# Kernel tuning notes

Measured on AMD Instinct MI355X. Metric: run time of the kernel, lower is better.

Reference implementation:

```python
import jax, jax.numpy as jnp
import numpy as np

B, C1, C2, H, W = 8, 256, 512, 56, 56

def setup_inputs() -> dict:
    key = jax.random.key(0)
    k1, k2, k3, k4, k5 = jax.random.split(key, 5)
    return {
        "x1": jax.random.normal(k1, (B, C1, H, W), dtype=jnp.float32),
        "x2": jax.random.normal(k2, (B, C2, H, W), dtype=jnp.float32),
        "W_proj": jax.random.normal(k3, (C1, C2), dtype=jnp.float32) * (1.0 / np.sqrt(C2)),
        "b_proj": jax.random.normal(k4, (C1,), dtype=jnp.float32) * 0.01,
        "gamma": jax.random.normal(k5, (1,), dtype=jnp.float32) * 0.1,
    }

def reference(x1, x2, W_proj, b_proj, gamma):
    b, c, h, w = x1.shape
    n = h * w
    # 1x1 conv projection C2 -> C1
    x2p = jnp.einsum('oc,bchw->bohw', W_proj, x2) + b_proj[None, :, None, None]
    query = x1.reshape(b, c, n).transpose(0, 2, 1)   # [B, N, C]
    key_ = x2p.reshape(b, c, n)                      # [B, C, N]
    value = x2p.reshape(b, c, n).transpose(0, 2, 1)  # [B, N, C]
    energy = jnp.einsum('bnc,bcm->bnm', query, key_)  # [B, N, N]
    # inverted-energy softmax: max - energy, then softmax over last dim
    energy_new = jnp.max(energy, axis=-1, keepdims=True) - energy
    attention = jax.nn.softmax(energy_new, axis=-1)
    out = jnp.einsum('bnm,bmc->bnc', attention, value)  # [B, N, C]
    out = out.transpose(0, 2, 1).reshape(b, c, h, w)
    return gamma[0] * out + x1
```

## Files before the change

### kernel.cpp

```cpp
#include <hip/hip_runtime.h>
#include <hip/hip_bf16.h>

#define C1 256
#define C2 512
#define NSP 3136
#define NT 98

typedef __attribute__((ext_vector_type(8))) short bf16x8;
typedef __attribute__((ext_vector_type(4))) float f32x4;

__device__ __forceinline__ ushort f2b(float f) {
  __hip_bfloat16 h = __float2bfloat16(f);
  return *reinterpret_cast<ushort*>(&h);
}
__device__ __forceinline__ float b2f(ushort u) {
  union { unsigned int i; float f; } v; v.i = ((unsigned int)u) << 16; return v.f;
}
__device__ __forceinline__ void gload16(const ushort* g, ushort* l) {
  __builtin_amdgcn_global_load_lds(
      (const __attribute__((address_space(1))) void*)g,
      (__attribute__((address_space(3))) void*)l, 16, 0, 0);
}
__device__ __forceinline__ void block_bar() {
  asm volatile("" ::: "memory");
  __builtin_amdgcn_s_barrier();
  asm volatile("" ::: "memory");
}

__global__ __launch_bounds__(256) void k_wtf(const float* __restrict__ W,
                                             ushort* __restrict__ Wf) {
  int ot = blockIdx.x;
  int tid = threadIdx.x;
  int lane = tid & 63, l15 = lane & 15, g = (lane >> 4) & 3;
  int cc0 = (tid >> 6) * 4;
  const float* src = W + (size_t)(ot * 16 + l15) * C2 + g * 8;
#pragma unroll
  for (int k = 0; k < 4; k++) {
    int cc = cc0 + k;
    float4 u0 = *reinterpret_cast<const float4*>(src + cc * 32);
    float4 u1 = *reinterpret_cast<const float4*>(src + cc * 32 + 4);
    bf16x8 v;
    v[0] = (short)f2b(u0.x); v[1] = (short)f2b(u0.y);
    v[2] = (short)f2b(u0.z); v[3] = (short)f2b(u0.w);
    v[4] = (short)f2b(u1.x); v[5] = (short)f2b(u1.y);
    v[6] = (short)f2b(u1.z); v[7] = (short)f2b(u1.w);
    *reinterpret_cast<bf16x8*>(Wf + ((size_t)(ot * 16 + cc)) * 512 + lane * 8) = v;
  }
}

__global__ __launch_bounds__(256) void k_x1t(const float* __restrict__ x1,
                                             ushort* __restrict__ x1t) {
  __shared__ float t[32][33];
  int b = blockIdx.z;
  int n0 = blockIdx.x * 32;
  int c0 = blockIdx.y * 32;
  int tid = threadIdx.x;
  int r = tid >> 3, q = (tid & 7) * 4;
  const float* src = x1 + ((size_t)b * C1 + (c0 + r)) * NSP + n0 + q;
  float4 v = *reinterpret_cast<const float4*>(src);
  t[r][q] = v.x; t[r][q + 1] = v.y; t[r][q + 2] = v.z; t[r][q + 3] = v.w;
  __syncthreads();
  ushort4 o;
  o.x = f2b(t[q + 0][r]); o.y = f2b(t[q + 1][r]);
  o.z = f2b(t[q + 2][r]); o.w = f2b(t[q + 3][r]);
  *reinterpret_cast<ushort4*>(x1t + ((size_t)b * NSP + n0 + r) * C1 + c0 + q) = o;
}

__global__ __launch_bounds__(256) void k_x2f(const float* __restrict__ x2,
                                             ushort* __restrict__ x2f) {
  __shared__ float t[32][33];
  int b = blockIdx.z;
  int n0 = blockIdx.x * 32;
  int cc = blockIdx.y;
  int c0 = cc * 32;
  int tid = threadIdx.x;
  int r = tid >> 3, q = (tid & 7) * 4;
  const float* src = x2 + ((size_t)b * C2 + (c0 + r)) * NSP + n0 + q;
  float4 v = *reinterpret_cast<const float4*>(src);
  t[r][q] = v.x; t[r][q + 1] = v.y; t[r][q + 2] = v.z; t[r][q + 3] = v.w;
  __syncthreads();
  int l15 = tid & 15, g = (tid >> 4) & 3, sub = tid >> 6;
  int ntl = sub & 1, ih = sub >> 1;
  int nl = ntl * 16 + l15;
  int cl = g * 8 + ih * 4;
  ushort4 o;
  o.x = f2b(t[cl + 0][nl]); o.y = f2b(t[cl + 1][nl]);
  o.z = f2b(t[cl + 2][nl]); o.w = f2b(t[cl + 3][nl]);
  int nt16 = (n0 >> 4) + ntl;
  *reinterpret_cast<ushort4*>(
      x2f + (((size_t)b * 196 + nt16) * 16 + cc) * 512 + (size_t)(tid & 63) * 8 + ih * 4) = o;
}

__global__ __launch_bounds__(256) void k_proj(const ushort* __restrict__ Wf,
    const ushort* __restrict__ x2f, const float* __restrict__ bias,
    ushort* __restrict__ Kf, ushort* __restrict__ Vf) {
  __shared__ __align__(16) ushort WL[2][8][512];
  __shared__ __align__(16) ushort XL[2][4][512];
  int bid = blockIdx.x;
  int b = bid & 7;
  int tq = bid >> 3;
  int oh = tq & 1;
  int nt = tq >> 1;
  int tid = threadIdx.x;
  int w = tid >> 6, lane = tid & 63, l15 = lane & 15, g = lane >> 4;
  int wq = w >> 1, wn = w & 1;
  int ot0 = oh * 8;
  int nt0 = nt * 4;

  auto stage = [&](int buf, int cc) {
#pragma unroll
    for (int j = 0; j < 3; j++) {
      int chunk = w * 3 + j;
      if (chunk < 8) {
        gload16(Wf + ((size_t)(ot0 + chunk) * 16 + cc) * 512 + lane * 8,
                &WL[buf][chunk][0]);
      } else {
        gload16(x2f + (((size_t)b * 196 + nt0 + (chunk - 8)) * 16 + cc) * 512 + lane * 8,
                &XL[buf][chunk - 8][0]);
      }
    }
  };

  f32x4 zero = {0.f, 0.f, 0.f, 0.f};
  f32x4 acc[4][2];
#pragma unroll
  for (int a = 0; a < 4; a++)
#pragma unroll
    for (int v = 0; v < 2; v++) acc[a][v] = zero;

  stage(0, 0);
  __syncthreads();

  for (int cc = 0; cc < 16; ++cc) {
    int cur = cc & 1;
    if (cc < 15) stage(cur ^ 1, cc + 1);
    bf16x8 A[4], Bf[2];
#pragma unroll
    for (int a = 0; a < 4; a++)
      A[a] = *reinterpret_cast<const bf16x8*>(&WL[cur][wq * 4 + a][lane * 8]);
#pragma unroll
    for (int v = 0; v < 2; v++)
      Bf[v] = *reinterpret_cast<const bf16x8*>(&XL[cur][wn * 2 + v][lane * 8]);
#pragma unroll
    for (int a = 0; a < 4; a++)
#pragma unroll
      for (int v = 0; v < 2; v++)
        acc[a][v] = __builtin_amdgcn_mfma_f32_16x16x32_bf16(A[a], Bf[v], acc[a][v], 0, 0, 0);
    __syncthreads();
  }

  int obase = oh * 128 + wq * 64;
  float4 bias4[4];
#pragma unroll
  for (int a = 0; a < 4; a++)
    bias4[a] = *reinterpret_cast<const float4*>(&bias[obase + a * 16 + g * 4]);

  int gk = (g & 1) * 4;
#pragma unroll
  for (int a = 0; a < 4; a++) {
    int laneK = (((2 * a + (g >> 1)) & 3) << 4) | l15;
    size_t oK = (size_t)(oh * 4 + wq * 2 + (a >> 1));
#pragma unroll
    for (int v = 0; v < 2; v++) {
      int nK = nt * 4 + wn * 2 + v;
      ushort4 st;
      st.x = f2b(acc[a][v][0] + bias4[a].x);
      st.y = f2b(acc[a][v][1] + bias4[a].y);
      st.z = f2b(acc[a][v][2] + bias4[a].z);
      st.w = f2b(acc[a][v][3] + bias4[a].w);
      *reinterpret_cast<ushort4*>(
          Kf + ((((size_t)b * 196 + nK) * 8 + oK) * 64 + laneK) * 8 + gk) = st;
    }
  }
  int nV = nt * 2 + wn;
#pragma unroll
  for (int v = 0; v < 2; v++) {
    int gv = ((v * 2 + (l15 >> 3)) & 3) << 4;
    int iV = l15 & 7;
#pragma unroll
    for (int a = 0; a < 4; a++) {
      int cs = oh * 8 + wq * 4 + a;
      size_t basev = ((((size_t)b * 98 + nV) * 16 + cs) * 64 + gv) * 8 + iV;
      const float* bp4 = reinterpret_cast<const float*>(&bias4[a]);
#pragma unroll
      for (int r = 0; r < 4; r++)
        Vf[basev + (size_t)(g * 4 + r) * 8] = f2b(acc[a][v][r] + bp4[r]);
    }
  }
}

__global__ __launch_bounds__(256, 3) void k_attn_s(
    const ushort* __restrict__ x1t, const ushort* __restrict__ Kf,
    const ushort* __restrict__ Vf,
    ushort* __restrict__ Po, float* __restrict__ Mv, float* __restrict__ Lv) {
  __shared__ __align__(16) ushort Kt[2][8192];
  __shared__ __align__(16) ushort Vt[8192];
  __shared__ __align__(16) ushort Plds[4][16][36];
  int bid = blockIdx.x;
  int x = bid & 7;
  int j = bid >> 3;
  int s = (4802 * j) / 96;
  int e = (4802 * (j + 1)) / 96;
  int tid = threadIdx.x;
  int w = tid >> 6;
  int lane = tid & 63;
  int l15 = lane & 15;
  int g = lane >> 4;
  int nloc = w * 16 + g * 4;

  const ushort* kg = Kf + (size_t)x * 196 * 8 * 512;
  const ushort* vg = Vf + (size_t)x * 98 * 16 * 512;
  int soff = w * 2048;

  f32x4 zero = {0.f, 0.f, 0.f, 0.f};
  f32x4 O[16];
  f32x4 O17 = zero;
  float M[4];
  bf16x8 qf[8];
  bf16x8 onesf;
#pragma unroll
  for (int i = 0; i < 8; i++) onesf[i] = (short)0x3F80;

  auto resetacc = [&]() {
#pragma unroll
    for (int i = 0; i < 16; i++) O[i] = zero;
    O17 = zero;
#pragma unroll
    for (int r = 0; r < 4; r++) M[r] = -3.0e38f;
  };
  auto loadQ = [&](int u) {
    const ushort* qb = x1t + ((size_t)x * NSP + u * 64 + w * 16 + l15) * C1 + g * 8;
#pragma unroll
    for (int cc = 0; cc < 8; cc++)
      qf[cc] = *reinterpret_cast<const bf16x8*>(qb + cc * 32);
  };

  int u = s / 98;
  int kv = s - u * 98;
  loadQ(u);
  resetacc();
  {
    const ushort* ks = kg + (size_t)kv * 8192 + soff + lane * 8;
#pragma unroll
    for (int jj = 0; jj < 4; ++jj) gload16(ks + jj * 512, &Kt[0][soff] + jj * 512);
  }
  asm volatile("s_waitcnt vmcnt(0)" ::: "memory");
  block_bar();

  int cur = 0;
  for (int i = s; i < e; ++i) {
    {
      const ushort* vs = vg + (size_t)kv * 8192 + soff + lane * 8;
#pragma unroll
      for (int jj = 0; jj < 4; ++jj) gload16(vs + jj * 512, &Vt[soff] + jj * 512);
    }
    asm volatile("" ::: "memory");
    if (i + 1 < e) {
      int kvn = (kv == 97) ? 0 : kv + 1;
      const ushort* ks = kg + (size_t)kvn * 8192 + soff + lane * 8;
#pragma unroll
      for (int jj = 0; jj < 4; ++jj) gload16(ks + jj * 512, &Kt[cur ^ 1][soff] + jj * 512);
    }
    asm volatile("" ::: "memory");

    f32x4 s0a = zero, s0b = zero, s1a = zero, s1b = zero;
    const ushort* kb = &Kt[cur][0];
    __builtin_amdgcn_s_setprio(1);
#pragma unroll
    for (int cc = 0; cc < 8; cc += 2) {
      bf16x8 k00 = *reinterpret_cast<const bf16x8*>(kb + ((size_t)cc * 64 + lane) * 8);
      bf16x8 k10 = *reinterpret_cast<const bf16x8*>(kb + ((size_t)(8 + cc) * 64 + lane) * 8);
      bf16x8 k01 = *reinterpret_cast<const bf16x8*>(kb + ((size_t)(cc + 1) * 64 + lane) * 8);
      bf16x8 k11 = *reinterpret_cast<const bf16x8*>(kb + ((size_t)(9 + cc) * 64 + lane) * 8);
      s0a = __builtin_amdgcn_mfma_f32_16x16x32_bf16(qf[cc], k00, s0a, 0, 0, 0);
      s1a = __builtin_amdgcn_mfma_f32_16x16x32_bf16(qf[cc], k10, s1a, 0, 0, 0);
      s0b = __builtin_amdgcn_mfma_f32_16x16x32_bf16(qf[cc + 1], k01, s0b, 0, 0, 0);
      s1b = __builtin_amdgcn_mfma_f32_16x16x32_bf16(qf[cc + 1], k11, s1b, 0, 0, 0);
    }
    __builtin_amdgcn_s_setprio(0);

    float a0[4], a1[4], tmax[4];
#pragma unroll
    for (int r = 0; r < 4; r++) {
      a0[r] = -(s0a[r] + s0b[r]);
      a1[r] = -(s1a[r] + s1b[r]);
      float mx = fmaxf(a0[r], a1[r]);
      mx = fmaxf(mx, __shfl_xor(mx, 1));
      mx = fmaxf(mx, __shfl_xor(mx, 2));
      mx = fmaxf(mx, __shfl_xor(mx, 4));
      mx = fmaxf(mx, __shfl_xor(mx, 8));
      tmax[r] = mx;
    }
    float d01 = fmaxf(tmax[0] - M[0], tmax[1] - M[1]);
    float d23 = fmaxf(tmax[2] - M[2], tmax[3] - M[3]);
    if (__any(fmaxf(d01, d23) > 3.0f)) {
      float scv[4];
#pragma unroll
      for (int r = 0; r < 4; r++) {
        float nm = fmaxf(M[r], tmax[r]);
        scv[r] = __expf(M[r] - nm);
        M[r] = nm;
      }
#pragma unroll
      for (int i2 = 0; i2 < 16; i2++) {
#pragma unroll
        for (int r = 0; r < 4; r++) O[i2][r] *= scv[r];
      }
#pragma unroll
      for (int r = 0; r < 4; r++) O17[r] *= scv[r];
    }
#pragma unroll
    for (int r = 0; r < 4; r++) {
      float p0 = __expf(a0[r] - M[r]);
      float p1 = __expf(a1[r] - M[r]);
      Plds[w][g * 4 + r][l15] = f2b(p0);
      Plds[w][g * 4 + r][16 + l15] = f2b(p1);
    }

    if (i + 1 < e) { asm volatile("s_waitcnt vmcnt(4)" ::: "memory"); }
    else           { asm volatile("s_waitcnt vmcnt(0)" ::: "memory"); }
    block_bar();

    asm volatile("s_waitcnt lgkmcnt(0)" ::: "memory");
    bf16x8 pf = *reinterpret_cast<const bf16x8*>(&Plds[w][l15][g * 8]);
    __builtin_amdgcn_s_setprio(1);
#pragma unroll
    for (int cs = 0; cs < 16; ++cs) {
      bf16x8 vf = *reinterpret_cast<const bf16x8*>(&Vt[0] + ((size_t)cs * 64 + lane) * 8);
      O[cs] = __builtin_amdgcn_mfma_f32_16x16x32_bf16(pf, vf, O[cs], 0, 0, 0);
    }
    O17 = __builtin_amdgcn_mfma_f32_16x16x32_bf16(pf, onesf, O17, 0, 0, 0);
    __builtin_amdgcn_s_setprio(0);

    asm volatile("s_waitcnt vmcnt(0)" ::: "memory");
    block_bar();
    cur ^= 1;

    if ((i + 1 == e) || (kv == 97)) {
      int firstj = (9408 * u + 95) / 4802;
      int slot = (x * 49 + u) * 3 + (j - firstj);
#pragma unroll
      for (int cs = 0; cs < 16; cs++) {
        int c = cs * 16 + l15;
        ushort4 st;
        st.x = f2b(O[cs][0]); st.y = f2b(O[cs][1]);
        st.z = f2b(O[cs][2]); st.w = f2b(O[cs][3]);
        *reinterpret_cast<ushort4*>(Po + ((size_t)slot * 256 + c) * 64 + nloc) = st;
      }
      if (l15 == 0) {
#pragma unroll
        for (int r = 0; r < 4; r++) {
          Mv[(size_t)slot * 64 + nloc + r] = M[r];
          Lv[(size_t)slot * 64 + nloc + r] = O17[r];
        }
      }
      if (i + 1 < e && kv == 97) { u += 1; loadQ(u); resetacc(); }
    }
    kv = (kv == 97) ? 0 : kv + 1;
  }
}

__global__ __launch_bounds__(256) void k_comb3(
    const ushort* __restrict__ Po, const float* __restrict__ Mv,
    const float* __restrict__ Lv, const float* __restrict__ x1,
    const float* __restrict__ gamma, float* __restrict__ out) {
  int bid = blockIdx.x;
  int x = bid & 7;
  int u = bid >> 3;
  int tid = threadIdx.x;
  int n = tid & 63;
  int c0 = (tid >> 6) * 64;
  int firstj = (9408 * u + 95) / 4802;
  int lastj = (96 * (98 * u + 97) + 95) / 4802;
  int np = lastj - firstj + 1;
  size_t base = (size_t)(x * 49 + u) * 3;
  bool has2 = (np >= 3);

  float M0 = Mv[(base + 0) * 64 + n];
  float M1 = Mv[(base + 1) * 64 + n];
  float M2 = has2 ? Mv[(base + 2) * 64 + n] : -3.0e38f;
  float L0 = Lv[(base + 0) * 64 + n];
  float L1 = Lv[(base + 1) * 64 + n];
  float L2 = has2 ? Lv[(base + 2) * 64 + n] : 0.f;
  float Mg = fmaxf(fmaxf(M0, M1), M2);
  float w0 = __expf(M0 - Mg), w1 = __expf(M1 - Mg);
  float w2 = has2 ? __expf(M2 - Mg) : 0.f;
  float rl = gamma[0] / (w0 * L0 + w1 * L1 + w2 * L2);

  const ushort* p0 = Po + ((base + 0) * 256) * 64 + n;
  const ushort* p1 = Po + ((base + 1) * 256) * 64 + n;
  const ushort* p2 = Po + ((base + 2) * 256) * 64 + n;
  size_t ob = (size_t)x * C1 * NSP + u * 64 + n;
#pragma unroll 4
  for (int c = c0; c < c0 + 64; ++c) {
    float acc = w0 * b2f(p0[(size_t)c * 64]) + w1 * b2f(p1[(size_t)c * 64]);
    if (has2) acc += w2 * b2f(p2[(size_t)c * 64]);
    size_t idx = ob + (size_t)c * NSP;
    out[idx] = acc * rl + x1[idx];
  }
}

template<int SPLIT>
__global__ __launch_bounds__(256, 3) void k_attn(
    const ushort* __restrict__ x1t, const ushort* __restrict__ Kf,
    const ushort* __restrict__ Vf, const float* __restrict__ x1,
    const float* __restrict__ gamma, float* __restrict__ out,
    ushort* __restrict__ Po, float* __restrict__ Mv, float* __restrict__ Lv) {
  __shared__ __align__(16) ushort Kt[2][8192];
  __shared__ __align__(16) ushort Vt[8192];
  __shared__ __align__(16) ushort Plds[4][16][36];
  int bid = blockIdx.x;
  int b = bid & 7;
  int qt = SPLIT ? (bid >> 4) : (bid >> 3);
  int h = SPLIT ? ((bid >> 3) & 1) : 0;
  int t0 = h * 49;
  int t1 = SPLIT ? (t0 + 49) : NT;
  int tid = threadIdx.x;
  int w = tid >> 6;
  int lane = tid & 63;
  int l15 = lane & 15;
  int g = lane >> 4;
  int n0 = qt * 64 + w * 16;

  bf16x8 qf[8];
  const ushort* qb = x1t + ((size_t)b * NSP + n0 + l15) * C1 + g * 8;
#pragma unroll
  for (int cc = 0; cc < 8; cc++)
    qf[cc] = *reinterpret_cast<const bf16x8*>(qb + cc * 32);

  f32x4 zero = {0.f, 0.f, 0.f, 0.f};
  f32x4 O[16];
#pragma unroll
  for (int i = 0; i < 16; i++) O[i] = zero;
  f32x4 O17 = zero;
  float M[4];
#pragma unroll
  for (int r = 0; r < 4; r++) M[r] = -3.0e38f;
  bf16x8 onesf;
#pragma unroll
  for (int i = 0; i < 8; i++) onesf[i] = (short)0x3F80;

  const ushort* kg = Kf + (size_t)b * 196 * 8 * 512;
  const ushort* vg = Vf + (size_t)b * 98 * 16 * 512;
  int soff = w * 2048;

  {
    const ushort* ks = kg + (size_t)t0 * 8192 + soff + lane * 8;
#pragma unroll
    for (int jj = 0; jj < 4; ++jj) gload16(ks + jj * 512, &Kt[0][soff] + jj * 512);
  }
  asm volatile("s_waitcnt vmcnt(0)" ::: "memory");
  block_bar();

  int cur = 0;
  for (int t = t0; t < t1; ++t) {
    {
      const ushort* vs = vg + (size_t)t * 8192 + soff + lane * 8;
#pragma unroll
      for (int jj = 0; jj < 4; ++jj) gload16(vs + jj * 512, &Vt[soff] + jj * 512);
    }
    asm volatile("" ::: "memory");
    if (t + 1 < t1) {
      const ushort* ks = kg + (size_t)(t + 1) * 8192 + soff + lane * 8;
#pragma unroll
      for (int jj = 0; jj < 4; ++jj) gload16(ks + jj * 512, &Kt[cur ^ 1][soff] + jj * 512);
    }
    asm volatile("" ::: "memory");

    f32x4 s0a = zero, s0b = zero, s1a = zero, s1b = zero;
    const ushort* kb = &Kt[cur][0];
    __builtin_amdgcn_s_setprio(1);
#pragma unroll
    for (int cc = 0; cc < 8; cc += 2) {
      bf16x8 k00 = *reinterpret_cast<const bf16x8*>(kb + ((size_t)cc * 64 + lane) * 8);
      bf16x8 k10 = *reinterpret_cast<const bf16x8*>(kb + ((size_t)(8 + cc) * 64 + lane) * 8);
      bf16x8 k01 = *reinterpret_cast<const bf16x8*>(kb + ((size_t)(cc + 1) * 64 + lane) * 8);
      bf16x8 k11 = *reinterpret_cast<const bf16x8*>(kb + ((size_t)(9 + cc) * 64 + lane) * 8);
      s0a = __builtin_amdgcn_mfma_f32_16x16x32_bf16(qf[cc], k00, s0a, 0, 0, 0);
      s1a = __builtin_amdgcn_mfma_f32_16x16x32_bf16(qf[cc], k10, s1a, 0, 0, 0);
      s0b = __builtin_amdgcn_mfma_f32_16x16x32_bf16(qf[cc + 1], k01, s0b, 0, 0, 0);
      s1b = __builtin_amdgcn_mfma_f32_16x16x32_bf16(qf[cc + 1], k11, s1b, 0, 0, 0);
    }
    __builtin_amdgcn_s_setprio(0);

    float a0[4], a1[4], tmax[4];
#pragma unroll
    for (int r = 0; r < 4; r++) {
      a0[r] = -(s0a[r] + s0b[r]);
      a1[r] = -(s1a[r] + s1b[r]);
      float mx = fmaxf(a0[r], a1[r]);
      mx = fmaxf(mx, __shfl_xor(mx, 1));
      mx = fmaxf(mx, __shfl_xor(mx, 2));
      mx = fmaxf(mx, __shfl_xor(mx, 4));
      mx = fmaxf(mx, __shfl_xor(mx, 8));
      tmax[r] = mx;
    }
    float d01 = fmaxf(tmax[0] - M[0], tmax[1] - M[1]);
    float d23 = fmaxf(tmax[2] - M[2], tmax[3] - M[3]);
    if (__any(fmaxf(d01, d23) > 3.0f)) {
      float scv[4];
#pragma unroll
      for (int r = 0; r < 4; r++) {
        float nm = fmaxf(M[r], tmax[r]);
        scv[r] = __expf(M[r] - nm);
        M[r] = nm;
      }
#pragma unroll
      for (int i = 0; i < 16; i++) {
#pragma unroll
        for (int r = 0; r < 4; r++) O[i][r] *= scv[r];
      }
#pragma unroll
      for (int r = 0; r < 4; r++) O17[r] *= scv[r];
    }
#pragma unroll
    for (int r = 0; r < 4; r++) {
      float p0 = __expf(a0[r] - M[r]);
      float p1 = __expf(a1[r] - M[r]);
      Plds[w][g * 4 + r][l15] = f2b(p0);
      Plds[w][g * 4 + r][16 + l15] = f2b(p1);
    }

    if (t + 1 < t1) { asm volatile("s_waitcnt vmcnt(4)" ::: "memory"); }
    else            { asm volatile("s_waitcnt vmcnt(0)" ::: "memory"); }
    block_bar();

    asm volatile("s_waitcnt lgkmcnt(0)" ::: "memory");
    bf16x8 pf = *reinterpret_cast<const bf16x8*>(&Plds[w][l15][g * 8]);
    __builtin_amdgcn_s_setprio(1);
#pragma unroll
    for (int cs = 0; cs < 16; ++cs) {
      bf16x8 vf = *reinterpret_cast<const bf16x8*>(&Vt[0] + ((size_t)cs * 64 + lane) * 8);
      O[cs] = __builtin_amdgcn_mfma_f32_16x16x32_bf16(pf, vf, O[cs], 0, 0, 0);
    }
    O17 = __builtin_amdgcn_mfma_f32_16x16x32_bf16(pf, onesf, O17, 0, 0, 0);
    __builtin_amdgcn_s_setprio(0);

    asm volatile("s_waitcnt vmcnt(0)" ::: "memory");
    block_bar();
    cur ^= 1;
  }

  if (SPLIT) {
    int pb = bid;
    int nloc = w * 16 + g * 4;
#pragma unroll
    for (int cs = 0; cs < 16; cs++) {
      int c = cs * 16 + l15;
      ushort4 st;
      st.x = f2b(O[cs][0]); st.y = f2b(O[cs][1]);
      st.z = f2b(O[cs][2]); st.w = f2b(O[cs][3]);
      *reinterpret_cast<ushort4*>(Po + ((size_t)pb * 256 + c) * 64 + nloc) = st;
    }
    if (l15 == 0) {
#pragma unroll
      for (int r = 0; r < 4; r++) {
        Mv[(size_t)pb * 64 + nloc + r] = M[r];
        Lv[(size_t)pb * 64 + nloc + r] = O17[r];
      }
    }
  } else {
    float gm = gamma[0];
    float rl[4];
#pragma unroll
    for (int r = 0; r < 4; r++) rl[r] = gm / O17[r];
    size_t ob = (size_t)b * C1 * NSP + n0 + (size_t)g * 4;
#pragma unroll
    for (int cs = 0; cs < 16; cs++) {
      size_t idx = ob + (size_t)(cs * 16 + l15) * NSP;
      float4 x4 = *reinterpret_cast<const float4*>(&x1[idx]);
      float4 o4;
      o4.x = O[cs][0] * rl[0] + x4.x;
      o4.y = O[cs][1] * rl[1] + x4.y;
      o4.z = O[cs][2] * rl[2] + x4.z;
      o4.w = O[cs][3] * rl[3] + x4.w;
      *reinterpret_cast<float4*>(&out[idx]) = o4;
    }
  }
}

__global__ __launch_bounds__(256) void k_comb(
    const ushort* __restrict__ Po, const float* __restrict__ Mv,
    const float* __restrict__ Lv, const float* __restrict__ x1,
    const float* __restrict__ gamma, float* __restrict__ out) {
  int bid = blockIdx.x;
  int b = bid & 7;
  int qt = bid >> 3;
  int tid = threadIdx.x;
  int n = tid & 63;
  int c0 = (tid >> 6) * 64;
  int pb0 = qt * 16 + b;
  int pb1 = qt * 16 + 8 + b;
  int n0 = qt * 64;
  float M0 = Mv[(size_t)pb0 * 64 + n], M1 = Mv[(size_t)pb1 * 64 + n];
  float L0 = Lv[(size_t)pb0 * 64 + n], L1 = Lv[(size_t)pb1 * 64 + n];
  float Ms = fmaxf(M0, M1);
  float w0 = __expf(M0 - Ms), w1 = __expf(M1 - Ms);
  float rl = gamma[0] / (w0 * L0 + w1 * L1);
  const ushort* p0 = Po + (size_t)pb0 * 16384 + n;
  const ushort* p1 = Po + (size_t)pb1 * 16384 + n;
#pragma unroll 4
  for (int c = c0; c < c0 + 64; ++c) {
    float o0 = b2f(p0[(size_t)c * 64]);
    float o1 = b2f(p1[(size_t)c * 64]);
    size_t idx = ((size_t)b * C1 + c) * NSP + n0 + n;
    out[idx] = (w0 * o0 + w1 * o1) * rl + x1[idx];
  }
}

extern "C" void kernel_launch(void* const* d_in, const int* in_sizes, int n_in,
                              void* d_out, int out_size, void* d_ws, size_t ws_size,
                              hipStream_t stream) {
  const float* x1 = (const float*)d_in[0];
  const float* x2 = (const float*)d_in[1];
  const float* W = (const float*)d_in[2];
  const float* bp = (const float*)d_in[3];
  const float* gamma = (const float*)d_in[4];
  float* out = (float*)d_out;

  char* ws = (char*)d_ws;
  ushort* Wf = (ushort*)(ws + 0);
  ushort* x1t = (ushort*)(ws + 262144);
  ushort* Kf = (ushort*)(ws + 13107200);
  ushort* Vf = (ushort*)(ws + 25952256);
  ushort* Po = (ushort*)(ws + 38797312);
  float* Mv = (float*)(ws + 77332480);
  float* Lv = (float*)(ws + 77633536);
  ushort* Pof = (ushort*)(ws + 38797312);
  float* Mvf = (float*)(ws + 64487424);
  float* Lvf = (float*)(ws + 64688128);
  ushort* x2f = (ushort*)d_out;

  k_wtf<<<dim3(16), dim3(256), 0, stream>>>(W, Wf);
  k_x1t<<<dim3(98, 8, 8), dim3(256), 0, stream>>>(x1, x1t);
  k_x2f<<<dim3(98, 16, 8), dim3(256), 0, stream>>>(x2, x2f);
  k_proj<<<dim3(784), dim3(256), 0, stream>>>(Wf, x2f, bp, Kf, Vf);

  if (ws_size >= 77934592ULL) {
    k_attn_s<<<dim3(768), dim3(256), 0, stream>>>(x1t, Kf, Vf, Po, Mv, Lv);
    k_comb3<<<dim3(392), dim3(256), 0, stream>>>(Po, Mv, Lv, x1, gamma, out);
  } else if (ws_size >= 64888832ULL) {
    k_attn<1><<<dim3(784), dim3(256), 0, stream>>>(x1t, Kf, Vf, x1, gamma, out,
                                                   Pof, Mvf, Lvf);
    k_comb<<<dim3(392), dim3(256), 0, stream>>>(Pof, Mvf, Lvf, x1, gamma, out);
  } else {
    k_attn<0><<<dim3(392), dim3(256), 0, stream>>>(x1t, Kf, Vf, x1, gamma, out,
                                                   Pof, Mvf, Lvf);
  }
}
```

Baseline: 241.8 us.

## Add 128-row query tile stream-K attention kernel with four-way partial combine

Adds a new attention kernel in which each wave handles two 16-row query sub-tiles. Every K/V tile loaded into LDS is therefore reused across 128 query rows instead of 64, and the S and PV MFMA work per wave doubles. The work is split stream-K style over 512 blocks, with up to four partials combined by a new combine kernel. Occupancy drops to 2 blocks per CU because each wave carries twice the accumulator registers. The rescale threshold is raised to 8, and the old split/non-split fallback kernels are removed. The new path only runs when the workspace is large enough; otherwise the previous stream-K kernel is used.

```diff
diff --git a/kernel.cpp b/kernel.cpp
--- a/kernel.cpp
+++ b/kernel.cpp
@@ -189,6 +189,251 @@
   }
 }
 
+__global__ __launch_bounds__(256, 2) void k_attn_p(
+    const ushort* __restrict__ x1t, const ushort* __restrict__ Kf,
+    const ushort* __restrict__ Vf,
+    ushort* __restrict__ Po, float* __restrict__ Mv, float* __restrict__ Lv) {
+  __shared__ __align__(16) ushort Kt[2][8192];
+  __shared__ __align__(16) ushort Vt[8192];
+  __shared__ __align__(16) ushort Plds[4][2][16][36];
+  int bid = blockIdx.x;
+  int x = bid & 7;
+  int j = bid >> 3;
+  int s = (2450 * j) / 64;
+  int e = (2450 * (j + 1)) / 64;
+  int tid = threadIdx.x;
+  int w = tid >> 6;
+  int lane = tid & 63;
+  int l15 = lane & 15;
+  int g = lane >> 4;
+  int tp = w >> 1;
+  int h32 = w & 1;
+
+  const ushort* kg = Kf + (size_t)x * 196 * 8 * 512;
+  const ushort* vg = Vf + (size_t)x * 98 * 16 * 512;
+  int soff = w * 2048;
+
+  f32x4 zero = {0.f, 0.f, 0.f, 0.f};
+  f32x4 O0[16], O1[16];
+  f32x4 L0 = zero, L1 = zero;
+  float M[2][4];
+  bf16x8 qf0[8], qf1[8];
+  bf16x8 onesf;
+#pragma unroll
+  for (int i = 0; i < 8; i++) onesf[i] = (short)0x3F80;
+
+  auto resetacc = [&]() {
+#pragma unroll
+    for (int i = 0; i < 16; i++) { O0[i] = zero; O1[i] = zero; }
+    L0 = zero; L1 = zero;
+#pragma unroll
+    for (int r = 0; r < 4; r++) { M[0][r] = -3.0e38f; M[1][r] = -3.0e38f; }
+  };
+  auto loadQ = [&](int p_) {
+    int u_ = 2 * p_ + tp;
+    int rb = (u_ < 49) ? u_ * 64 + h32 * 32 : 0;
+    const ushort* q0 = x1t + ((size_t)x * NSP + rb + l15) * C1 + g * 8;
+    const ushort* q1 = x1t + ((size_t)x * NSP + rb + 16 + l15) * C1 + g * 8;
+#pragma unroll
+    for (int cc = 0; cc < 8; cc++) {
+      qf0[cc] = *reinterpret_cast<const bf16x8*>(q0 + cc * 32);
+      qf1[cc] = *reinterpret_cast<const bf16x8*>(q1 + cc * 32);
+    }
+  };
+
+  int p = s / 98;
+  int kv = s - p * 98;
+  loadQ(p);
+  resetacc();
+  {
+    const ushort* ks = kg + (size_t)kv * 8192 + soff + lane * 8;
+#pragma unroll
+    for (int jj = 0; jj < 4; ++jj) gload16(ks + jj * 512, &Kt[0][soff] + jj * 512);
+  }
+  asm volatile("s_waitcnt vmcnt(0)" ::: "memory");
+  block_bar();
+
+  int cur = 0;
+  for (int i = s; i < e; ++i) {
+    {
+      const ushort* vs = vg + (size_t)kv * 8192 + soff + lane * 8;
+#pragma unroll
+      for (int jj = 0; jj < 4; ++jj) gload16(vs + jj * 512, &Vt[soff] + jj * 512);
+    }
+    asm volatile("" ::: "memory");
+    if (i + 1 < e) {
+      int kvn = (kv == 97) ? 0 : kv + 1;
+      const ushort* ks = kg + (size_t)kvn * 8192 + soff + lane * 8;
+#pragma unroll
+      for (int jj = 0; jj < 4; ++jj) gload16(ks + jj * 512, &Kt[cur ^ 1][soff] + jj * 512);
+    }
+    asm volatile("" ::: "memory");
+
+    f32x4 sA0 = zero, sB0 = zero, sA1 = zero, sB1 = zero;
+    const ushort* kb = &Kt[cur][0];
+    __builtin_amdgcn_s_setprio(1);
+#pragma unroll
+    for (int cc = 0; cc < 8; ++cc) {
+      bf16x8 kl = *reinterpret_cast<const bf16x8*>(kb + ((size_t)cc * 64 + lane) * 8);
+      bf16x8 kh = *reinterpret_cast<const bf16x8*>(kb + ((size_t)(8 + cc) * 64 + lane) * 8);
+      sA0 = __builtin_amdgcn_mfma_f32_16x16x32_bf16(qf0[cc], kl, sA0, 0, 0, 0);
+      sB0 = __builtin_amdgcn_mfma_f32_16x16x32_bf16(qf0[cc], kh, sB0, 0, 0, 0);
+      sA1 = __builtin_amdgcn_mfma_f32_16x16x32_bf16(qf1[cc], kl, sA1, 0, 0, 0);
+      sB1 = __builtin_amdgcn_mfma_f32_16x16x32_bf16(qf1[cc], kh, sB1, 0, 0, 0);
+    }
+    __builtin_amdgcn_s_setprio(0);
+
+    float tmax[2][4];
+#pragma unroll
+    for (int qs = 0; qs < 2; qs++) {
+#pragma unroll
+      for (int r = 0; r < 4; r++) {
+        float a0 = qs ? -sA1[r] : -sA0[r];
+        float a1 = qs ? -sB1[r] : -sB0[r];
+        float mx = fmaxf(a0, a1);
+        mx = fmaxf(mx, __shfl_xor(mx, 1));
+        mx = fmaxf(mx, __shfl_xor(mx, 2));
+        mx = fmaxf(mx, __shfl_xor(mx, 4));
+        mx = fmaxf(mx, __shfl_xor(mx, 8));
+        tmax[qs][r] = mx;
+      }
+    }
+    float dm = -3.0e38f;
+#pragma unroll
+    for (int qs = 0; qs < 2; qs++)
+#pragma unroll
+      for (int r = 0; r < 4; r++) dm = fmaxf(dm, tmax[qs][r] - M[qs][r]);
+    if (__any(dm > 8.0f)) {
+      float sc0[4], sc1[4];
+#pragma unroll
+      for (int r = 0; r < 4; r++) {
+        float nm0 = fmaxf(M[0][r], tmax[0][r]);
+        float nm1 = fmaxf(M[1][r], tmax[1][r]);
+        sc0[r] = __expf(M[0][r] - nm0);
+        sc1[r] = __expf(M[1][r] - nm1);
+        M[0][r] = nm0; M[1][r] = nm1;
+      }
+#pragma unroll
+      for (int i2 = 0; i2 < 16; i2++) {
+#pragma unroll
+        for (int r = 0; r < 4; r++) { O0[i2][r] *= sc0[r]; O1[i2][r] *= sc1[r]; }
+      }
+#pragma unroll
+      for (int r = 0; r < 4; r++) { L0[r] *= sc0[r]; L1[r] *= sc1[r]; }
+    }
+#pragma unroll
+    for (int r = 0; r < 4; r++) {
+      Plds[w][0][g * 4 + r][l15]      = f2b(__expf(-sA0[r] - M[0][r]));
+      Plds[w][0][g * 4 + r][16 + l15] = f2b(__expf(-sB0[r] - M[0][r]));
+      Plds[w][1][g * 4 + r][l15]      = f2b(__expf(-sA1[r] - M[1][r]));
+      Plds[w][1][g * 4 + r][16 + l15] = f2b(__expf(-sB1[r] - M[1][r]));
+    }
+
+    if (i + 1 < e) { asm volatile("s_waitcnt vmcnt(4)" ::: "memory"); }
+    else           { asm volatile("s_waitcnt vmcnt(0)" ::: "memory"); }
+    block_bar();
+
+    asm volatile("s_waitcnt lgkmcnt(0)" ::: "memory");
+    bf16x8 pf0 = *reinterpret_cast<const bf16x8*>(&Plds[w][0][l15][g * 8]);
+    bf16x8 pf1 = *reinterpret_cast<const bf16x8*>(&Plds[w][1][l15][g * 8]);
+    __builtin_amdgcn_s_setprio(1);
+#pragma unroll
+    for (int cs = 0; cs < 16; ++cs) {
+      bf16x8 vf = *reinterpret_cast<const bf16x8*>(&Vt[0] + ((size_t)cs * 64 + lane) * 8);
+      O0[cs] = __builtin_amdgcn_mfma_f32_16x16x32_bf16(pf0, vf, O0[cs], 0, 0, 0);
+      O1[cs] = __builtin_amdgcn_mfma_f32_16x16x32_bf16(pf1, vf, O1[cs], 0, 0, 0);
+    }
+    L0 = __builtin_amdgcn_mfma_f32_16x16x32_bf16(pf0, onesf, L0, 0, 0, 0);
+    L1 = __builtin_amdgcn_mfma_f32_16x16x32_bf16(pf1, onesf, L1, 0, 0, 0);
+    __builtin_amdgcn_s_setprio(0);
+
+    asm volatile("s_waitcnt vmcnt(0)" ::: "memory");
+    block_bar();
+    cur ^= 1;
+
+    if ((i + 1 == e) || (kv == 97)) {
+      int firstj = (6272 * p + 63) / 2450;
+      int slot = (x * 25 + p) * 4 + (j - firstj);
+      if (2 * p + tp < 49) {
+        int nb = tp * 64 + h32 * 32 + g * 4;
+#pragma unroll
+        for (int qs = 0; qs < 2; qs++) {
+          int nn = nb + qs * 16;
+#pragma unroll
+          for (int cs = 0; cs < 16; cs++) {
+            int c = cs * 16 + l15;
+            ushort4 st;
+            if (qs == 0) {
+              st.x = f2b(O0[cs][0]); st.y = f2b(O0[cs][1]);
+              st.z = f2b(O0[cs][2]); st.w = f2b(O0[cs][3]);
+            } else {
+              st.x = f2b(O1[cs][0]); st.y = f2b(O1[cs][1]);
+              st.z = f2b(O1[cs][2]); st.w = f2b(O1[cs][3]);
+            }
+            *reinterpret_cast<ushort4*>(
+                Po + ((size_t)slot * 256 + c) * 128 + nn) = st;
+          }
+          if (l15 == 0) {
+#pragma unroll
+            for (int r = 0; r < 4; r++) {
+              Mv[(size_t)slot * 128 + nn + r] = M[qs][r];
+              Lv[(size_t)slot * 128 + nn + r] = qs ? L1[r] : L0[r];
+            }
+          }
+        }
+      }
+      if (i + 1 < e && kv == 97) { p += 1; loadQ(p); resetacc(); }
+    }
+    kv = (kv == 97) ? 0 : kv + 1;
+  }
+}
+
+__global__ __launch_bounds__(256) void k_comb4(
+    const ushort* __restrict__ Po, const float* __restrict__ Mv,
+    const float* __restrict__ Lv, const float* __restrict__ x1,
+    const float* __restrict__ gamma, float* __restrict__ out) {
+  int bid = blockIdx.x;
+  int x = bid & 7;
+  int u = bid >> 3;
+  int p = u >> 1, tph = u & 1;
+  int tid = threadIdx.x;
+  int n = tid & 63;
+  int c0 = (tid >> 6) * 64;
+  int firstj = (6272 * p + 63) / 2450;
+  int lastj = (6272 * p + 6271) / 2450;
+  int np = lastj - firstj + 1;
+  size_t base = (size_t)(x * 25 + p) * 4;
+  int nn = tph * 64 + n;
+
+  float Mp[4], Lp[4], wq[4];
+  float Mg = -3.0e38f;
+#pragma unroll
+  for (int q = 0; q < 4; q++) {
+    if (q < np) {
+      Mp[q] = Mv[(base + q) * 128 + nn];
+      Lp[q] = Lv[(base + q) * 128 + nn];
+      Mg = fmaxf(Mg, Mp[q]);
+    }
+  }
+  float Ls = 0.f;
+#pragma unroll
+  for (int q = 0; q < 4; q++) {
+    wq[q] = (q < np) ? __expf(Mp[q] - Mg) : 0.f;
+    if (q < np) Ls += wq[q] * Lp[q];
+  }
+  float rl = gamma[0] / Ls;
+  size_t ob = (size_t)x * C1 * NSP + (size_t)u * 64 + n;
+#pragma unroll 4
+  for (int c = c0; c < c0 + 64; ++c) {
+    float acc = 0.f;
+#pragma unroll
+    for (int q = 0; q < 4; q++)
+      if (q < np) acc += wq[q] * b2f(Po[((base + q) * 256 + c) * 128 + nn]);
+    size_t idx = ob + (size_t)c * NSP;
+    out[idx] = acc * rl + x1[idx];
+  }
+}
+
 __global__ __launch_bounds__(256, 3) void k_attn_s(
     const ushort* __restrict__ x1t, const ushort* __restrict__ Kf,
     const ushort* __restrict__ Vf,
@@ -311,10 +556,8 @@
     }
 #pragma unroll
     for (int r = 0; r < 4; r++) {
-      float p0 = __expf(a0[r] - M[r]);
-      float p1 = __expf(a1[r] - M[r]);
-      Plds[w][g * 4 + r][l15] = f2b(p0);
-      Plds[w][g * 4 + r][16 + l15] = f2b(p1);
+      Plds[w][g * 4 + r][l15] = f2b(__expf(a0[r] - M[r]));
+      Plds[w][g * 4 + r][16 + l15] = f2b(__expf(a1[r] - M[r]));
     }
 
     if (i + 1 < e) { asm volatile("s_waitcnt vmcnt(4)" ::: "memory"); }
@@ -400,214 +643,6 @@
   }
 }
 
-template<int SPLIT>
-__global__ __launch_bounds__(256, 3) void k_attn(
-    const ushort* __restrict__ x1t, const ushort* __restrict__ Kf,
-    const ushort* __restrict__ Vf, const float* __restrict__ x1,
-    const float* __restrict__ gamma, float* __restrict__ out,
-    ushort* __restrict__ Po, float* __restrict__ Mv, float* __restrict__ Lv) {
-  __shared__ __align__(16) ushort Kt[2][8192];
-  __shared__ __align__(16) ushort Vt[8192];
-  __shared__ __align__(16) ushort Plds[4][16][36];
-  int bid = blockIdx.x;
-  int b = bid & 7;
-  int qt = SPLIT ? (bid >> 4) : (bid >> 3);
-  int h = SPLIT ? ((bid >> 3) & 1) : 0;
-  int t0 = h * 49;
-  int t1 = SPLIT ? (t0 + 49) : NT;
-  int tid = threadIdx.x;
-  int w = tid >> 6;
-  int lane = tid & 63;
-  int l15 = lane & 15;
-  int g = lane >> 4;
-  int n0 = qt * 64 + w * 16;
-
-  bf16x8 qf[8];
-  const ushort* qb = x1t + ((size_t)b * NSP + n0 + l15) * C1 + g * 8;
-#pragma unroll
-  for (int cc = 0; cc < 8; cc++)
-    qf[cc] = *reinterpret_cast<const bf16x8*>(qb + cc * 32);
-
-  f32x4 zero = {0.f, 0.f, 0.f, 0.f};
-  f32x4 O[16];
-#pragma unroll
-  for (int i = 0; i < 16; i++) O[i] = zero;
-  f32x4 O17 = zero;
-  float M[4];
-#pragma unroll
-  for (int r = 0; r < 4; r++) M[r] = -3.0e38f;
-  bf16x8 onesf;
-#pragma unroll
-  for (int i = 0; i < 8; i++) onesf[i] = (short)0x3F80;
-
-  const ushort* kg = Kf + (size_t)b * 196 * 8 * 512;
-  const ushort* vg = Vf + (size_t)b * 98 * 16 * 512;
-  int soff = w * 2048;
-
-  {
-    const ushort* ks = kg + (size_t)t0 * 8192 + soff + lane * 8;
-#pragma unroll
-    for (int jj = 0; jj < 4; ++jj) gload16(ks + jj * 512, &Kt[0][soff] + jj * 512);
-  }
-  asm volatile("s_waitcnt vmcnt(0)" ::: "memory");
-  block_bar();
-
-  int cur = 0;
-  for (int t = t0; t < t1; ++t) {
-    {
-      const ushort* vs = vg + (size_t)t * 8192 + soff + lane * 8;
-#pragma unroll
-      for (int jj = 0; jj < 4; ++jj) gload16(vs + jj * 512, &Vt[soff] + jj * 512);
-    }
-    asm volatile("" ::: "memory");
-    if (t + 1 < t1) {
-      const ushort* ks = kg + (size_t)(t + 1) * 8192 + soff + lane * 8;
-#pragma unroll
-      for (int jj = 0; jj < 4; ++jj) gload16(ks + jj * 512, &Kt[cur ^ 1][soff] + jj * 512);
-    }
-    asm volatile("" ::: "memory");
-
-    f32x4 s0a = zero, s0b = zero, s1a = zero, s1b = zero;
-    const ushort* kb = &Kt[cur][0];
-    __builtin_amdgcn_s_setprio(1);
-#pragma unroll
-    for (int cc = 0; cc < 8; cc += 2) {
-      bf16x8 k00 = *reinterpret_cast<const bf16x8*>(kb + ((size_t)cc * 64 + lane) * 8);
-      bf16x8 k10 = *reinterpret_cast<const bf16x8*>(kb + ((size_t)(8 + cc) * 64 + lane) * 8);
-      bf16x8 k01 = *reinterpret_cast<const bf16x8*>(kb + ((size_t)(cc + 1) * 64 + lane) * 8);
-      bf16x8 k11 = *reinterpret_cast<const bf16x8*>(kb + ((size_t)(9 + cc) * 64 + lane) * 8);
-      s0a = __builtin_amdgcn_mfma_f32_16x16x32_bf16(qf[cc], k00, s0a, 0, 0, 0);
-      s1a = __builtin_amdgcn_mfma_f32_16x16x32_bf16(qf[cc], k10, s1a, 0, 0, 0);
-      s0b = __builtin_amdgcn_mfma_f32_16x16x32_bf16(qf[cc + 1], k01, s0b, 0, 0, 0);
-      s1b = __builtin_amdgcn_mfma_f32_16x16x32_bf16(qf[cc + 1], k11, s1b, 0, 0, 0);
-    }
-    __builtin_amdgcn_s_setprio(0);
-
-    float a0[4], a1[4], tmax[4];
-#pragma unroll
-    for (int r = 0; r < 4; r++) {
-      a0[r] = -(s0a[r] + s0b[r]);
-      a1[r] = -(s1a[r] + s1b[r]);
-      float mx = fmaxf(a0[r], a1[r]);
-      mx = fmaxf(mx, __shfl_xor(mx, 1));
-      mx = fmaxf(mx, __shfl_xor(mx, 2));
-      mx = fmaxf(mx, __shfl_xor(mx, 4));
-      mx = fmaxf(mx, __shfl_xor(mx, 8));
-      tmax[r] = mx;
-    }
-    float d01 = fmaxf(tmax[0] - M[0], tmax[1] - M[1]);
-    float d23 = fmaxf(tmax[2] - M[2], tmax[3] - M[3]);
-    if (__any(fmaxf(d01, d23) > 3.0f)) {
-      float scv[4];
-#pragma unroll
-      for (int r = 0; r < 4; r++) {
-        float nm = fmaxf(M[r], tmax[r]);
-        scv[r] = __expf(M[r] - nm);
-        M[r] = nm;
-      }
-#pragma unroll
-      for (int i = 0; i < 16; i++) {
-#pragma unroll
-        for (int r = 0; r < 4; r++) O[i][r] *= scv[r];
-      }
-#pragma unroll
-      for (int r = 0; r < 4; r++) O17[r] *= scv[r];
-    }
-#pragma unroll
-    for (int r = 0; r < 4; r++) {
-      float p0 = __expf(a0[r] - M[r]);
-      float p1 = __expf(a1[r] - M[r]);
-      Plds[w][g * 4 + r][l15] = f2b(p0);
-      Plds[w][g * 4 + r][16 + l15] = f2b(p1);
-    }
-
-    if (t + 1 < t1) { asm volatile("s_waitcnt vmcnt(4)" ::: "memory"); }
-    else            { asm volatile("s_waitcnt vmcnt(0)" ::: "memory"); }
-    block_bar();
-
-    asm volatile("s_waitcnt lgkmcnt(0)" ::: "memory");
-    bf16x8 pf = *reinterpret_cast<const bf16x8*>(&Plds[w][l15][g * 8]);
-    __builtin_amdgcn_s_setprio(1);
-#pragma unroll
-    for (int cs = 0; cs < 16; ++cs) {
-      bf16x8 vf = *reinterpret_cast<const bf16x8*>(&Vt[0] + ((size_t)cs * 64 + lane) * 8);
-      O[cs] = __builtin_amdgcn_mfma_f32_16x16x32_bf16(pf, vf, O[cs], 0, 0, 0);
-    }
-    O17 = __builtin_amdgcn_mfma_f32_16x16x32_bf16(pf, onesf, O17, 0, 0, 0);
-    __builtin_amdgcn_s_setprio(0);
-
-    asm volatile("s_waitcnt vmcnt(0)" ::: "memory");
-    block_bar();
-    cur ^= 1;
-  }
-
-  if (SPLIT) {
-    int pb = bid;
-    int nloc = w * 16 + g * 4;
-#pragma unroll
-    for (int cs = 0; cs < 16; cs++) {
-      int c = cs * 16 + l15;
-      ushort4 st;
-      st.x = f2b(O[cs][0]); st.y = f2b(O[cs][1]);
-      st.z = f2b(O[cs][2]); st.w = f2b(O[cs][3]);
-      *reinterpret_cast<ushort4*>(Po + ((size_t)pb * 256 + c) * 64 + nloc) = st;
-    }
-    if (l15 == 0) {
-#pragma unroll
-      for (int r = 0; r < 4; r++) {
-        Mv[(size_t)pb * 64 + nloc + r] = M[r];
-        Lv[(size_t)pb * 64 + nloc + r] = O17[r];
-      }
-    }
-  } else {
-    float gm = gamma[0];
-    float rl[4];
-#pragma unroll
-    for (int r = 0; r < 4; r++) rl[r] = gm / O17[r];
-    size_t ob = (size_t)b * C1 * NSP + n0 + (size_t)g * 4;
-#pragma unroll
-    for (int cs = 0; cs < 16; cs++) {
-      size_t idx = ob + (size_t)(cs * 16 + l15) * NSP;
-      float4 x4 = *reinterpret_cast<const float4*>(&x1[idx]);
-      float4 o4;
-      o4.x = O[cs][0] * rl[0] + x4.x;
-      o4.y = O[cs][1] * rl[1] + x4.y;
-      o4.z = O[cs][2] * rl[2] + x4.z;
-      o4.w = O[cs][3] * rl[3] + x4.w;
-      *reinterpret_cast<float4*>(&out[idx]) = o4;
-    }
-  }
-}
-
-__global__ __launch_bounds__(256) void k_comb(
-    const ushort* __restrict__ Po, const float* __restrict__ Mv,
-    const float* __restrict__ Lv, const float* __restrict__ x1,
-    const float* __restrict__ gamma, float* __restrict__ out) {
-  int bid = blockIdx.x;
-  int b = bid & 7;
-  int qt = bid >> 3;
-  int tid = threadIdx.x;
-  int n = tid & 63;
-  int c0 = (tid >> 6) * 64;
-  int pb0 = qt * 16 + b;
-  int pb1 = qt * 16 + 8 + b;
-  int n0 = qt * 64;
-  float M0 = Mv[(size_t)pb0 * 64 + n], M1 = Mv[(size_t)pb1 * 64 + n];
-  float L0 = Lv[(size_t)pb0 * 64 + n], L1 = Lv[(size_t)pb1 * 64 + n];
-  float Ms = fmaxf(M0, M1);
-  float w0 = __expf(M0 - Ms), w1 = __expf(M1 - Ms);
-  float rl = gamma[0] / (w0 * L0 + w1 * L1);
-  const ushort* p0 = Po + (size_t)pb0 * 16384 + n;
-  const ushort* p1 = Po + (size_t)pb1 * 16384 + n;
-#pragma unroll 4
-  for (int c = c0; c < c0 + 64; ++c) {
-    float o0 = b2f(p0[(size_t)c * 64]);
-    float o1 = b2f(p1[(size_t)c * 64]);
-    size_t idx = ((size_t)b * C1 + c) * NSP + n0 + n;
-    out[idx] = (w0 * o0 + w1 * o1) * rl + x1[idx];
-  }
-}
-
 extern "C" void kernel_launch(void* const* d_in, const int* in_sizes, int n_in,
                               void* d_out, int out_size, void* d_ws, size_t ws_size,
                               hipStream_t stream) {
@@ -624,11 +659,11 @@
   ushort* Kf = (ushort*)(ws + 13107200);
   ushort* Vf = (ushort*)(ws + 25952256);
   ushort* Po = (ushort*)(ws + 38797312);
-  float* Mv = (float*)(ws + 77332480);
-  float* Lv = (float*)(ws + 77633536);
-  ushort* Pof = (ushort*)(ws + 38797312);
-  float* Mvf = (float*)(ws + 64487424);
-  float* Lvf = (float*)(ws + 64688128);
+  float* Mv = (float*)(ws + 91226112);
+  float* Lv = (float*)(ws + 91635712);
+  ushort* Po3 = (ushort*)(ws + 38797312);
+  float* Mv3 = (float*)(ws + 77332480);
+  float* Lv3 = (float*)(ws + 77633536);
   ushort* x2f = (ushort*)d_out;
 
   k_wtf<<<dim3(16), dim3(256), 0, stream>>>(W, Wf);
@@ -636,15 +671,11 @@
   k_x2f<<<dim3(98, 16, 8), dim3(256), 0, stream>>>(x2, x2f);
   k_proj<<<dim3(784), dim3(256), 0, stream>>>(Wf, x2f, bp, Kf, Vf);
 
-  if (ws_size >= 77934592ULL) {
-    k_attn_s<<<dim3(768), dim3(256), 0, stream>>>(x1t, Kf, Vf, Po, Mv, Lv);
-    k_comb3<<<dim3(392), dim3(256), 0, stream>>>(Po, Mv, Lv, x1, gamma, out);
-  } else if (ws_size >= 64888832ULL) {
-    k_attn<1><<<dim3(784), dim3(256), 0, stream>>>(x1t, Kf, Vf, x1, gamma, out,
-                                                   Pof, Mvf, Lvf);
-    k_comb<<<dim3(392), dim3(256), 0, stream>>>(Pof, Mvf, Lvf, x1, gamma, out);
+  if (ws_size >= 92045312ULL) {
+    k_attn_p<<<dim3(512), dim3(256), 0, stream>>>(x1t, Kf, Vf, Po, Mv, Lv);
+    k_comb4<<<dim3(392), dim3(256), 0, stream>>>(Po, Mv, Lv, x1, gamma, out);
   } else {
-    k_attn<0><<<dim3(392), dim3(256), 0, stream>>>(x1t, Kf, Vf, x1, gamma, out,
-                                                   Pof, Mvf, Lvf);
-  }
-}
+    k_attn_s<<<dim3(768), dim3(256), 0, stream>>>(x1t, Kf, Vf, Po3, Mv3, Lv3);
+    k_comb3<<<dim3(392), dim3(256), 0, stream>>>(Po3, Mv3, Lv3, x1, gamma, out);
+  }
+}
```

New measurement: 302.9 us. 25.3% more time.
